# Kernel tuning notes

Measured on AMD Instinct MI355X. Metric: run time of the kernel, lower is better.

Reference implementation:

```python
import jax, jax.numpy as jnp
import numpy as np

N = 100_000   # total nodes in batch
E = 800_000   # total edges (avg degree ~8)
D = 128       # emb_dim
B = 1024      # graphs per batch
NT = 10       # num_tasks
EV = 4        # edge-type vocab
L_ENC = 5     # encoder GNN layers
L_RAT = 2     # rationale GNN layers
GAMMA = 0.4
BN_EPS = 1e-5


def setup_inputs() -> dict:
    keys = iter(jax.random.split(jax.random.key(0), 64))

    def nrm(shape, s=0.05):
        return jax.random.normal(next(keys), shape, jnp.float32) * s

    inp = {}
    inp["x"] = jax.random.normal(next(keys), (N, 4), jnp.float32)
    inp["edge_index"] = jax.random.randint(next(keys), (2, E), 0, N, jnp.int32)
    inp["edge_attr"] = jax.random.randint(next(keys), (E,), 0, EV, jnp.int32)
    inp["batch"] = jnp.sort(jax.random.randint(next(keys), (N,), 0, B, jnp.int32))
    inp["num_graphs"] = B
    u = jax.random.uniform(next(keys), (N, 2), jnp.float32, 1e-6, 1.0 - 1e-6)
    inp["gumbels"] = -jnp.log(-jnp.log(u))  # Gumbel(0,1) noise for gumbel_softmax

    inp["node_W"] = nrm((4, D)); inp["node_b"] = jnp.zeros((D,), jnp.float32)

    def gnn_params(L, pre):
        inp[pre + "eps"] = jnp.zeros((L,), jnp.float32)
        inp[pre + "edge"] = nrm((L, EV, D))
        inp[pre + "W1"] = nrm((L, D, 2 * D)); inp[pre + "b1"] = jnp.zeros((L, 2 * D), jnp.float32)
        inp[pre + "bn1g"] = jnp.ones((L, 2 * D), jnp.float32); inp[pre + "bn1b"] = jnp.zeros((L, 2 * D), jnp.float32)
        inp[pre + "W2"] = nrm((L, 2 * D, D)); inp[pre + "b2"] = jnp.zeros((L, D), jnp.float32)
        inp[pre + "bng"] = jnp.ones((L, D), jnp.float32); inp[pre + "bnb"] = jnp.zeros((L, D), jnp.float32)

    gnn_params(L_ENC, "enc_")
    gnn_params(L_RAT, "rat_")

    inp["gate_W1"] = nrm((D, 2 * D)); inp["gate_b1"] = jnp.zeros((2 * D,), jnp.float32)
    inp["gate_bng"] = jnp.ones((2 * D,), jnp.float32); inp["gate_bnb"] = jnp.zeros((2 * D,), jnp.float32)
    inp["gate_W2"] = nrm((2 * D, 2)); inp["gate_b2"] = jnp.zeros((2,), jnp.float32)

    inp["pred_W1"] = nrm((D, 2 * D)); inp["pred_b1"] = jnp.zeros((2 * D,), jnp.float32)
    inp["pred_bng"] = jnp.ones((2 * D,), jnp.float32); inp["pred_bnb"] = jnp.zeros((2 * D,), jnp.float32)
    inp["pred_W2"] = nrm((2 * D, NT)); inp["pred_b2"] = jnp.zeros((NT,), jnp.float32)
    return inp


def _bn(x, g, b):
    # training-mode BatchNorm1d: batch statistics over dim 0
    m = x.mean(0)
    v = x.var(0)
    return (x - m) * jax.lax.rsqrt(v + BN_EPS) * g + b


def _gin_stack(h, src, dst, ea, eps, edge, W1, b1, bn1g, bn1b, W2, b2, bng, bnb):
    # OGB-style GIN with edge embeddings, outer BN, residual
    n = h.shape[0]
    L = eps.shape[0]
    for l in range(L):
        msg = jax.nn.relu(h[src] + edge[l][ea])                 # [E, D] gather
        aggr = jax.ops.segment_sum(msg, dst, num_segments=n)    # scatter-add
        z = (1.0 + eps[l]) * h + aggr
        z = jax.nn.relu(_bn(z @ W1[l] + b1[l], bn1g[l], bn1b[l])) @ W2[l] + b2[l]
        z = _bn(z, bng[l], bnb[l])
        if l < L - 1:
            z = jax.nn.relu(z)
        h = z + h                                               # residual
    return h


def reference(x, gumbels, node_W, node_b,
              enc_eps, enc_edge, enc_W1, enc_b1, enc_bn1g, enc_bn1b, enc_W2, enc_b2, enc_bng, enc_bnb,
              rat_eps, rat_edge, rat_W1, rat_b1, rat_bn1g, rat_bn1b, rat_W2, rat_b2, rat_bng, rat_bnb,
              gate_W1, gate_b1, gate_bng, gate_bnb, gate_W2, gate_b2,
              pred_W1, pred_b1, pred_bng, pred_bnb, pred_W2, pred_b2,
              edge_index, edge_attr, batch, num_graphs):
    src, dst = edge_index[0], edge_index[1]
    h0 = x @ node_W + node_b                                    # node_enoder
    h_node = _gin_stack(h0, src, dst, edge_attr, enc_eps, enc_edge, enc_W1, enc_b1,
                        enc_bn1g, enc_bn1b, enc_W2, enc_b2, enc_bng, enc_bnb)
    xr = _gin_stack(h0, src, dst, edge_attr, rat_eps, rat_edge, rat_W1, rat_b1,
                    rat_bn1g, rat_bn1b, rat_W2, rat_b2, rat_bng, rat_bnb)

    # gate_nn: Linear -> BN -> ReLU -> (Dropout, eval) -> Linear
    logits = jax.nn.relu(_bn(xr @ gate_W1 + gate_b1, gate_bng, gate_bnb)) @ gate_W2 + gate_b2

    # F.gumbel_softmax(hard=True, tau=1) with straight-through estimator
    y_soft = jax.nn.softmax(logits + gumbels, axis=-1)
    y_hard = jax.nn.one_hot(jnp.argmax(y_soft, axis=-1), 2, dtype=y_soft.dtype)
    y = y_hard + y_soft - jax.lax.stop_gradient(y_soft)
    gate = y[:, 1:2]                                            # [N, 1]

    ones = jnp.ones((x.shape[0],), x.dtype)
    counts = jnp.maximum(jax.ops.segment_sum(ones, batch, num_segments=num_graphs), 1.0)[:, None]
    h_r = jax.ops.segment_sum(gate * h_node, batch, num_segments=num_graphs) / counts
    r_num = jax.ops.segment_sum(gate, batch, num_segments=num_graphs) + 1e-8
    env_num = jax.ops.segment_sum(1.0 - gate, batch, num_segments=num_graphs) + 1e-8

    pred_rem = jax.nn.relu(_bn(h_r @ pred_W1 + pred_b1, pred_bng, pred_bnb)) @ pred_W2 + pred_b2
    loss_reg = jnp.abs(r_num / (r_num + env_num) - GAMMA).mean()
    return pred_rem, loss_reg
```

## Files before the change

kernel.cpp:

```cpp
#include <hip/hip_runtime.h>
#include <cstddef>

#define DIM    128
#define DIM2   256
#define NGRAPH 1024
#define NTASK  10
#define NEV    4
#define BNEPS  1e-5f
#define GAMMA_ 0.4f

typedef __attribute__((ext_vector_type(4))) float f32x4;
typedef __attribute__((ext_vector_type(8))) short s16x8;

static __device__ __forceinline__ float relu_(float v) { return v > 0.f ? v : 0.f; }
static __device__ __forceinline__ unsigned short f2b(float f) {
    unsigned int u = __float_as_uint(f);
    unsigned int r = (u + 0x7fffu + ((u >> 16) & 1u)) >> 16;
    return (unsigned short)r;
}
static __device__ __forceinline__ float b2f(unsigned short b) {
    return __uint_as_float(((unsigned int)b) << 16);
}
static __device__ __forceinline__ unsigned int pk(float a, float b) {
    return (unsigned int)f2b(a) | ((unsigned int)f2b(b) << 16);
}

__global__ void k_count_deg(const int* __restrict__ dst, int* __restrict__ deg, int E) {
    int e = blockIdx.x * blockDim.x + threadIdx.x;
    if (e < E) atomicAdd(&deg[dst[e]], 1);
}

__global__ void k_scan_block(const int* __restrict__ deg, int* __restrict__ incl,
                             int* __restrict__ bsum, int n) {
    __shared__ int s[1024];
    int i = blockIdx.x * 1024 + threadIdx.x;
    int v = (i < n) ? deg[i] : 0;
    s[threadIdx.x] = v;
    __syncthreads();
    for (int off = 1; off < 1024; off <<= 1) {
        int t = (threadIdx.x >= off) ? s[threadIdx.x - off] : 0;
        __syncthreads();
        s[threadIdx.x] += t;
        __syncthreads();
    }
    if (i < n) incl[i] = s[threadIdx.x];
    if (threadIdx.x == 1023) bsum[blockIdx.x] = s[1023];
}

__global__ void k_scan_bsum(const int* __restrict__ bsum, int* __restrict__ boff, int nb) {
    __shared__ int s[128];
    int t = threadIdx.x;
    s[t] = (t < nb) ? bsum[t] : 0;
    __syncthreads();
    for (int off = 1; off < 128; off <<= 1) {
        int v = (t >= off) ? s[t - off] : 0;
        __syncthreads();
        s[t] += v;
        __syncthreads();
    }
    if (t < nb) boff[t] = (t == 0) ? 0 : s[t - 1];
}

__global__ void k_scan_final(const int* __restrict__ incl, const int* __restrict__ deg,
                             const int* __restrict__ boff, int* __restrict__ rowptr,
                             int* __restrict__ cursor, int n) {
    int i = blockIdx.x * blockDim.x + threadIdx.x;
    if (i < n) {
        int v = incl[i] + boff[i >> 10];
        rowptr[i + 1] = v;
        cursor[i] = v - deg[i];
    }
    if (i == 0) rowptr[0] = 0;
}

__global__ void k_fill_csr(const int* __restrict__ src, const int* __restrict__ dst,
                           const int* __restrict__ ea, int* __restrict__ cursor,
                           int* __restrict__ src_s, int* __restrict__ ea_s, int E) {
    int e = blockIdx.x * blockDim.x + threadIdx.x;
    if (e < E) {
        int p = atomicAdd(&cursor[dst[e]], 1);
        src_s[p] = src[e];
        ea_s[p]  = ea[e];
    }
}

__global__ void k_graph_ptr(const int* __restrict__ batch, int* __restrict__ gptr, int n, int B) {
    int g = blockIdx.x * blockDim.x + threadIdx.x;
    if (g > B) return;
    int lo = 0, hi = n;
    while (lo < hi) {
        int mid = (lo + hi) >> 1;
        if (batch[mid] < g) lo = mid + 1; else hi = mid;
    }
    gptr[g] = lo;
}

__global__ void k_wconv(const float* __restrict__ W, unsigned short* __restrict__ Wt,
                        int L, int K, int COUT) {
    long long i = (long long)blockIdx.x * 256 + threadIdx.x;
    long long total = (long long)L * K * COUT;
    if (i >= total) return;
    int l = (int)(i / (K * COUT));
    int rem = (int)(i % (K * COUT));
    int c = rem / K, k = rem % K;
    Wt[i] = f2b(W[(size_t)l * K * COUT + (size_t)k * COUT + c]);
}

__global__ void k_h0(const float* __restrict__ x, const float* __restrict__ W,
                     const float* __restrict__ b, float* __restrict__ h,
                     unsigned short* __restrict__ hb, int n) {
    int idx = blockIdx.x * blockDim.x + threadIdx.x;
    if (idx >= n * (DIM / 4)) return;
    int node = idx >> 5;
    int c4 = (idx & 31) << 2;
    const float* xr = x + (size_t)node * 4;
    float x0 = xr[0], x1 = xr[1], x2 = xr[2], x3 = xr[3];
    const float4 w0 = *(const float4*)(W + c4);
    const float4 w1 = *(const float4*)(W + DIM + c4);
    const float4 w2 = *(const float4*)(W + 2 * DIM + c4);
    const float4 w3 = *(const float4*)(W + 3 * DIM + c4);
    const float4 bv = *(const float4*)(b + c4);
    float4 o;
    o.x = bv.x + x0 * w0.x + x1 * w1.x + x2 * w2.x + x3 * w3.x;
    o.y = bv.y + x0 * w0.y + x1 * w1.y + x2 * w2.y + x3 * w3.y;
    o.z = bv.z + x0 * w0.z + x1 * w1.z + x2 * w2.z + x3 * w3.z;
    o.w = bv.w + x0 * w0.w + x1 * w1.w + x2 * w2.w + x3 * w3.w;
    size_t off = (size_t)node * DIM + c4;
    *(float4*)(h + off) = o;
    if (hb) {
        uint2 ob;
        ob.x = pk(o.x, o.y);
        ob.y = pk(o.z, o.w);
        *(uint2*)(hb + off) = ob;
    }
}

__global__ __launch_bounds__(256) void k_aggregate(
    const float* __restrict__ h, const int* __restrict__ rowptr,
    const int* __restrict__ src_s, const int* __restrict__ ea_s,
    const float* __restrict__ emb, const float* __restrict__ eps_arr, int l,
    float* __restrict__ zout, int n) {
    __shared__ float semb[NEV * DIM];
    int t = threadIdx.x;
    for (int i = t; i < NEV * DIM; i += 256) semb[i] = emb[(size_t)l * NEV * DIM + i];
    __syncthreads();
    int grp = t >> 5, lane = t & 31;
    int node = blockIdx.x * 8 + grp;
    if (node >= n) return;
    float eps1 = 1.0f + eps_arr[l];
    int beg = rowptr[node], end = rowptr[node + 1];
    int c = lane << 2;
    float4 acc = {0.f, 0.f, 0.f, 0.f};
    for (int e = beg; e < end; ++e) {
        int s = src_s[e];
        int a = ea_s[e];
        const float4 hv = *(const float4*)(h + (size_t)s * DIM + c);
        const float4 ev = *(const float4*)(semb + a * DIM + c);
        acc.x += relu_(hv.x + ev.x);
        acc.y += relu_(hv.y + ev.y);
        acc.z += relu_(hv.z + ev.z);
        acc.w += relu_(hv.w + ev.w);
    }
    const float4 hn = *(const float4*)(h + (size_t)node * DIM + c);
    float4 o;
    o.x = eps1 * hn.x + acc.x;
    o.y = eps1 * hn.y + acc.y;
    o.z = eps1 * hn.z + acc.z;
    o.w = eps1 * hn.w + acc.w;
    *(float4*)(zout + (size_t)node * DIM + c) = o;
}

__global__ __launch_bounds__(256) void k_agg_bf(
    const unsigned short* __restrict__ hb, const int* __restrict__ rowptr,
    const int* __restrict__ src_s, const int* __restrict__ ea_s,
    const float* __restrict__ emb, const float* __restrict__ eps_arr, int l,
    unsigned short* __restrict__ zb, int n) {
    __shared__ float semb[NEV * DIM];
    int t = threadIdx.x;
    for (int i = t; i < NEV * DIM; i += 256) semb[i] = emb[(size_t)l * NEV * DIM + i];
    __syncthreads();
    int grp = t >> 5, lane = t & 31;
    int node = blockIdx.x * 8 + grp;
    if (node >= n) return;
    float eps1 = 1.0f + eps_arr[l];
    int beg = rowptr[node], end = rowptr[node + 1];
    int c = lane << 2;
    float ax = 0.f, ay = 0.f, az = 0.f, aw = 0.f;
    for (int e = beg; e < end; ++e) {
        int s = src_s[e];
        int a = ea_s[e];
        ushort4 hv = *(const ushort4*)(hb + (size_t)s * DIM + c);
        const float4 ev = *(const float4*)(semb + a * DIM + c);
        ax += relu_(b2f(hv.x) + ev.x);
        ay += relu_(b2f(hv.y) + ev.y);
        az += relu_(b2f(hv.z) + ev.z);
        aw += relu_(b2f(hv.w) + ev.w);
    }
    ushort4 hn = *(const ushort4*)(hb + (size_t)node * DIM + c);
    uint2 o;
    o.x = pk(eps1 * b2f(hn.x) + ax, eps1 * b2f(hn.y) + ay);
    o.y = pk(eps1 * b2f(hn.z) + az, eps1 * b2f(hn.w) + aw);
    *(uint2*)(zb + (size_t)node * DIM + c) = o;
}

template <int K, int COUT, bool TRANS, bool STATS>
__global__ __launch_bounds__(256) void k_mmf(
    const float* __restrict__ A, const float* __restrict__ W,
    const float* __restrict__ bias, const float* __restrict__ scl,
    const float* __restrict__ shf, float* __restrict__ C,
    float* __restrict__ psum, float* __restrict__ psq, int nrows) {
    __shared__ float Asl[64][36];
    __shared__ float Wsl[32][132];
    const int t = threadIdx.x;
    const int row0 = blockIdx.x * 64;
    const int col0 = blockIdx.y * 128;
    const int tc = t & 15;
    const int tr = t >> 4;
    float4 acc[4][2] = {};
    for (int k0 = 0; k0 < K; k0 += 32) {
#pragma unroll
        for (int j = 0; j < 2; ++j) {
            int ff = j * 256 + t;
            int r = ff >> 3;
            int kc = (ff & 7) << 2;
            int grow = row0 + r;
            float4 v = {0.f, 0.f, 0.f, 0.f};
            if (grow < nrows) v = *(const float4*)(A + (size_t)grow * K + (k0 + kc));
            if (TRANS) {
                const float4 s4 = *(const float4*)(scl + k0 + kc);
                const float4 h4 = *(const float4*)(shf + k0 + kc);
                v.x = relu_(v.x * s4.x + h4.x);
                v.y = relu_(v.y * s4.y + h4.y);
                v.z = relu_(v.z * s4.z + h4.z);
                v.w = relu_(v.w * s4.w + h4.w);
            }
            *(float4*)(&Asl[r][kc]) = v;
        }
#pragma unroll
        for (int j = 0; j < 4; ++j) {
            int ff = j * 256 + t;
            int kr = ff >> 5;
            int cc = (ff & 31) << 2;
            float4 wv = *(const float4*)(W + (size_t)(k0 + kr) * COUT + (col0 + cc));
            *(float4*)(&Wsl[kr][cc]) = wv;
        }
        __syncthreads();
#pragma unroll
        for (int k4 = 0; k4 < 32; k4 += 4) {
            f32x4 a4[4];
#pragma unroll
            for (int r = 0; r < 4; ++r)
                a4[r] = *(const f32x4*)(&Asl[(tr << 2) + r][k4]);
#pragma unroll
            for (int kk = 0; kk < 4; ++kk) {
                const float4 w0 = *(const float4*)(&Wsl[k4 + kk][tc << 2]);
                const float4 w1 = *(const float4*)(&Wsl[k4 + kk][64 + (tc << 2)]);
                const float a0 = a4[0][kk];
                const float a1 = a4[1][kk];
                const float a2 = a4[2][kk];
                const float a3 = a4[3][kk];
                acc[0][0].x += a0 * w0.x; acc[0][0].y += a0 * w0.y; acc[0][0].z += a0 * w0.z; acc[0][0].w += a0 * w0.w;
                acc[0][1].x += a0 * w1.x; acc[0][1].y += a0 * w1.y; acc[0][1].z += a0 * w1.z; acc[0][1].w += a0 * w1.w;
                acc[1][0].x += a1 * w0.x; acc[1][0].y += a1 * w0.y; acc[1][0].z += a1 * w0.z; acc[1][0].w += a1 * w0.w;
                acc[1][1].x += a1 * w1.x; acc[1][1].y += a1 * w1.y; acc[1][1].z += a1 * w1.z; acc[1][1].w += a1 * w1.w;
                acc[2][0].x += a2 * w0.x; acc[2][0].y += a2 * w0.y; acc[2][0].z += a2 * w0.z; acc[2][0].w += a2 * w0.w;
                acc[2][1].x += a2 * w1.x; acc[2][1].y += a2 * w1.y; acc[2][1].z += a2 * w1.z; acc[2][1].w += a2 * w1.w;
                acc[3][0].x += a3 * w0.x; acc[3][0].y += a3 * w0.y; acc[3][0].z += a3 * w0.z; acc[3][0].w += a3 * w0.w;
                acc[3][1].x += a3 * w1.x; acc[3][1].y += a3 * w1.y; acc[3][1].z += a3 * w1.z; acc[3][1].w += a3 * w1.w;
            }
        }
        __syncthreads();
    }
    const float4 b0 = *(const float4*)(bias + col0 + (tc << 2));
    const float4 b1 = *(const float4*)(bias + col0 + 64 + (tc << 2));
    float s0[4] = {}, q0[4] = {}, s1[4] = {}, q1[4] = {};
#pragma unroll
    for (int r = 0; r < 4; ++r) {
        int row = row0 + (tr << 2) + r;
        if (row < nrows) {
            float4 o0, o1;
            o0.x = acc[r][0].x + b0.x; o0.y = acc[r][0].y + b0.y;
            o0.z = acc[r][0].z + b0.z; o0.w = acc[r][0].w + b0.w;
            o1.x = acc[r][1].x + b1.x; o1.y = acc[r][1].y + b1.y;
            o1.z = acc[r][1].z + b1.z; o1.w = acc[r][1].w + b1.w;
            *(float4*)(C + (size_t)row * COUT + col0 + (tc << 2)) = o0;
            *(float4*)(C + (size_t)row * COUT + col0 + 64 + (tc << 2)) = o1;
            if (STATS) {
                s0[0] += o0.x; q0[0] += o0.x * o0.x;  s0[1] += o0.y; q0[1] += o0.y * o0.y;
                s0[2] += o0.z; q0[2] += o0.z * o0.z;  s0[3] += o0.w; q0[3] += o0.w * o0.w;
                s1[0] += o1.x; q1[0] += o1.x * o1.x;  s1[1] += o1.y; q1[1] += o1.y * o1.y;
                s1[2] += o1.z; q1[2] += o1.z * o1.z;  s1[3] += o1.w; q1[3] += o1.w * o1.w;
            }
        }
    }
    if (STATS) {
        float* ls1 = &Wsl[0][0];
        float* ls2 = &Asl[0][0];
        __syncthreads();
#pragma unroll
        for (int j = 0; j < 4; ++j) {
            ls1[tr * 132 + (tc << 2) + j] = s0[j];
            ls1[tr * 132 + 64 + (tc << 2) + j] = s1[j];
            ls2[tr * 132 + (tc << 2) + j] = q0[j];
            ls2[tr * 132 + 64 + (tc << 2) + j] = q1[j];
        }
        __syncthreads();
        if (t < 128) {
            float ss = 0.f, qq = 0.f;
#pragma unroll
            for (int g = 0; g < 16; ++g) { ss += ls1[g * 132 + t]; qq += ls2[g * 132 + t]; }
            psum[(size_t)blockIdx.x * COUT + col0 + t] = ss;
            psq[(size_t)blockIdx.x * COUT + col0 + t]  = qq;
        }
    }
}

template <int K, int COUT, bool TRANS, bool OUT_BF, bool STATS>
__global__ __launch_bounds__(256) void k_mm_bf(
    const unsigned short* __restrict__ A, const unsigned short* __restrict__ Wt,
    const float* __restrict__ bias, const float* __restrict__ scl,
    const float* __restrict__ shf, void* __restrict__ Cout,
    float* __restrict__ psum, float* __restrict__ psq, int nrows) {
    __shared__ unsigned short As[128 * 64];
    __shared__ unsigned short Bs[64 * 64];
    const int t = threadIdx.x;
    const int row0 = blockIdx.x * 128;
    const int col0 = blockIdx.y * 64;
    const int wid = t >> 6, lane = t & 63;
    const int wm = wid & 1, wn = wid >> 1;
    const int lr = lane & 15, lk = lane >> 4;
    f32x4 acc[4][2] = {};
    for (int k0 = 0; k0 < K; k0 += 64) {
#pragma unroll
        for (int i = 0; i < 4; ++i) {
            int idx = i * 256 + t;
            int r = idx >> 3;
            int kc = (idx & 7) * 8;
            int gr = row0 + r;
            uint4 v = {0u, 0u, 0u, 0u};
            if (!TRANS) {
                if (gr < nrows) v = *(const uint4*)(A + (size_t)gr * K + k0 + kc);
            } else {
                if (gr < nrows) {
                    uint4 raw = *(const uint4*)(A + (size_t)gr * K + k0 + kc);
                    const float4 s0 = *(const float4*)(scl + k0 + kc);
                    const float4 s1 = *(const float4*)(scl + k0 + kc + 4);
                    const float4 h0 = *(const float4*)(shf + k0 + kc);
                    const float4 h1 = *(const float4*)(shf + k0 + kc + 4);
                    float v0 = relu_(b2f((unsigned short)(raw.x & 0xffff)) * s0.x + h0.x);
                    float v1 = relu_(b2f((unsigned short)(raw.x >> 16))    * s0.y + h0.y);
                    float v2 = relu_(b2f((unsigned short)(raw.y & 0xffff)) * s0.z + h0.z);
                    float v3 = relu_(b2f((unsigned short)(raw.y >> 16))    * s0.w + h0.w);
                    float v4 = relu_(b2f((unsigned short)(raw.z & 0xffff)) * s1.x + h1.x);
                    float v5 = relu_(b2f((unsigned short)(raw.z >> 16))    * s1.y + h1.y);
                    float v6 = relu_(b2f((unsigned short)(raw.w & 0xffff)) * s1.z + h1.z);
                    float v7 = relu_(b2f((unsigned short)(raw.w >> 16))    * s1.w + h1.w);
                    v.x = pk(v0, v1); v.y = pk(v2, v3); v.z = pk(v4, v5); v.w = pk(v6, v7);
                }
            }
            int byte = (r * 128 + kc * 2) ^ ((r & 7) << 4);
            *(uint4*)((char*)As + byte) = v;
        }
#pragma unroll
        for (int i = 0; i < 2; ++i) {
            int idx = i * 256 + t;
            int c = idx >> 3;
            int kc = (idx & 7) * 8;
            uint4 v = *(const uint4*)(Wt + (size_t)(col0 + c) * K + k0 + kc);
            int byte = (c * 128 + kc * 2) ^ ((c & 7) << 4);
            *(uint4*)((char*)Bs + byte) = v;
        }
        __syncthreads();
#pragma unroll
        for (int kk = 0; kk < 64; kk += 32) {
            s16x8 bfrag[2];
#pragma unroll
            for (int n = 0; n < 2; ++n) {
                int c = wn * 32 + n * 16 + lr;
                int byte = (c * 128 + (kk + lk * 8) * 2) ^ ((c & 7) << 4);
                bfrag[n] = *(const s16x8*)((const char*)Bs + byte);
            }
#pragma unroll
            for (int m = 0; m < 4; ++m) {
                int r = wm * 64 + m * 16 + lr;
                int byte = (r * 128 + (kk + lk * 8) * 2) ^ ((r & 7) << 4);
                s16x8 afrag = *(const s16x8*)((const char*)As + byte);
                acc[m][0] = __builtin_amdgcn_mfma_f32_16x16x32_bf16(afrag, bfrag[0], acc[m][0], 0, 0, 0);
                acc[m][1] = __builtin_amdgcn_mfma_f32_16x16x32_bf16(afrag, bfrag[1], acc[m][1], 0, 0, 0);
            }
        }
        __syncthreads();
    }
    float* ls1 = (float*)&Bs[0];
    float* ls2 = ls1 + 512;
#pragma unroll
    for (int n = 0; n < 2; ++n) {
        int col_local = wn * 32 + n * 16 + lr;
        int col = col0 + col_local;
        float bv = bias[col];
        float s = 0.f, q = 0.f;
#pragma unroll
        for (int m = 0; m < 4; ++m) {
#pragma unroll
            for (int j = 0; j < 4; ++j) {
                int row = row0 + wm * 64 + m * 16 + lk * 4 + j;
                if (row < nrows) {
                    float v = acc[m][n][j] + bv;
                    if (OUT_BF)
                        ((unsigned short*)Cout)[(size_t)row * COUT + col] = f2b(v);
                    else
                        ((float*)Cout)[(size_t)row * COUT + col] = v;
                    if (STATS) { s += v; q += v * v; }
                }
            }
        }
        if (STATS) {
            ls1[col_local * 8 + wm * 4 + lk] = s;
            ls2[col_local * 8 + wm * 4 + lk] = q;
        }
    }
    if (STATS) {
        __syncthreads();
        if (t < 64) {
            float ss = 0.f, qq = 0.f;
#pragma unroll
            for (int g = 0; g < 8; ++g) { ss += ls1[t * 8 + g]; qq += ls2[t * 8 + g]; }
            psum[(size_t)blockIdx.x * COUT + col0 + t] = ss;
            psq[(size_t)blockIdx.x * COUT + col0 + t]  = qq;
        }
    }
}

__global__ void k_stats_fin(const float* __restrict__ psum, const float* __restrict__ psq,
                            const float* __restrict__ g, const float* __restrict__ bta,
                            float* __restrict__ scl, float* __restrict__ shf,
                            int nrows, int C, int P) {
    __shared__ float r1[256], r2[256];
    int c = blockIdx.x;
    int t = threadIdx.x;
    float s = 0.f, sq = 0.f;
    for (int b = t; b < P; b += 256) {
        s  += psum[(size_t)b * C + c];
        sq += psq[(size_t)b * C + c];
    }
    r1[t] = s; r2[t] = sq;
    for (int off = 128; off; off >>= 1) {
        __syncthreads();
        if (t < off) { r1[t] += r1[t + off]; r2[t] += r2[t + off]; }
    }
    __syncthreads();
    if (t == 0) {
        float mean = r1[0] / (float)nrows;
        float var  = r2[0] / (float)nrows - mean * mean;
        float is   = rsqrtf(var + BNEPS);
        float sc   = g[c] * is;
        scl[c] = sc;
        shf[c] = bta[c] - mean * sc;
    }
}

__global__ void k_residual(const float* __restrict__ z, const float* __restrict__ scl,
                           const float* __restrict__ shf, float* __restrict__ h,
                           unsigned short* __restrict__ hb, int n, int relu_flag) {
    int idx = blockIdx.x * blockDim.x + threadIdx.x;
    if (idx >= n * (DIM / 4)) return;
    int i = idx * 4;
    int c = i & 127;
    const float4 zv = *(const float4*)(z + i);
    const float4 sv = *(const float4*)(scl + c);
    const float4 fv = *(const float4*)(shf + c);
    float4 hv = *(const float4*)(h + i);
    float v0 = zv.x * sv.x + fv.x;
    float v1 = zv.y * sv.y + fv.y;
    float v2 = zv.z * sv.z + fv.z;
    float v3 = zv.w * sv.w + fv.w;
    if (relu_flag) { v0 = relu_(v0); v1 = relu_(v1); v2 = relu_(v2); v3 = relu_(v3); }
    float4 o;
    o.x = v0 + hv.x; o.y = v1 + hv.y; o.z = v2 + hv.z; o.w = v3 + hv.w;
    *(float4*)(h + i) = o;
    if (hb) {
        uint2 ob;
        ob.x = pk(o.x, o.y);
        ob.y = pk(o.z, o.w);
        *(uint2*)(hb + i) = ob;
    }
}

__global__ __launch_bounds__(256) void k_gate(
    const float* __restrict__ t1, const float* __restrict__ scl, const float* __restrict__ shf,
    const float* __restrict__ W2, const float* __restrict__ b2,
    const float* __restrict__ gumbels, float* __restrict__ gate, int n) {
    __shared__ float w0[256], w1[256];
    int t = threadIdx.x;
    w0[t] = W2[t * 2];
    w1[t] = W2[t * 2 + 1];
    __syncthreads();
    int wv = t >> 6, lane = t & 63;
    int node = blockIdx.x * 4 + wv;
    if (node >= n) return;
    int c = lane << 2;
    const float4 v = *(const float4*)(t1 + (size_t)node * 256 + c);
    float a0 = 0.f, a1 = 0.f;
    float tv;
    tv = relu_(v.x * scl[c + 0] + shf[c + 0]); a0 += tv * w0[c + 0]; a1 += tv * w1[c + 0];
    tv = relu_(v.y * scl[c + 1] + shf[c + 1]); a0 += tv * w0[c + 1]; a1 += tv * w1[c + 1];
    tv = relu_(v.z * scl[c + 2] + shf[c + 2]); a0 += tv * w0[c + 2]; a1 += tv * w1[c + 2];
    tv = relu_(v.w * scl[c + 3] + shf[c + 3]); a0 += tv * w0[c + 3]; a1 += tv * w1[c + 3];
    for (int off = 32; off; off >>= 1) {
        a0 += __shfl_down(a0, off);
        a1 += __shfl_down(a1, off);
    }
    if (lane == 0) {
        float l0 = a0 + b2[0] + gumbels[(size_t)node * 2 + 0];
        float l1 = a1 + b2[1] + gumbels[(size_t)node * 2 + 1];
        gate[node] = (l1 > l0) ? 1.f : 0.f;
    }
}

__global__ void k_segreduce(const float* __restrict__ h, const float* __restrict__ gate,
                            const int* __restrict__ gptr, float* __restrict__ hr,
                            float* __restrict__ lossg, int B) {
    __shared__ float red[256];
    int g = blockIdx.x, t = threadIdx.x;
    int beg = gptr[g], end = gptr[g + 1];
    int cnt = end - beg;
    float gs = 0.f;
    for (int nrow = beg + t; nrow < end; nrow += 256) gs += gate[nrow];
    red[t] = gs;
    for (int off = 128; off; off >>= 1) {
        __syncthreads();
        if (t < off) red[t] += red[t + off];
    }
    __syncthreads();
    float rnum = red[0];
    __syncthreads();
    if (t == 0) {
        float r = rnum + 1e-8f;
        float e = ((float)cnt - rnum) + 1e-8f;
        lossg[g] = fabsf(r / (r + e) - GAMMA_);
    }
    int c = t & 127, rs = t >> 7;
    float acc = 0.f;
    for (int nrow = beg + rs; nrow < end; nrow += 2) {
        float gt = gate[nrow];
        if (gt != 0.f) acc += h[(size_t)nrow * 128 + c];
    }
    red[t] = acc;
    __syncthreads();
    if (rs == 0) {
        float tot = red[t] + red[t + 128];
        hr[(size_t)g * 128 + c] = tot / fmaxf((float)cnt, 1.f);
    }
}

__global__ void k_loss(const float* __restrict__ lossg, float* __restrict__ out, int B) {
    __shared__ float red[256];
    int t = threadIdx.x;
    float s = 0.f;
    for (int g = t; g < B; g += 256) s += lossg[g];
    red[t] = s;
    for (int off = 128; off; off >>= 1) {
        __syncthreads();
        if (t < off) red[t] += red[t + off];
    }
    __syncthreads();
    if (t == 0) out[NGRAPH * NTASK] = red[0] / (float)B;
}

__global__ void k_pred_out(const float* __restrict__ tp, const float* __restrict__ scl,
                           const float* __restrict__ shf, const float* __restrict__ W2,
                           const float* __restrict__ b2, float* __restrict__ out, int B) {
    int i = blockIdx.x * blockDim.x + threadIdx.x;
    if (i >= B * NTASK) return;
    int g = i / NTASK, j = i % NTASK;
    float acc = b2[j];
    for (int k = 0; k < 256; ++k) {
        float v = relu_(tp[(size_t)g * 256 + k] * scl[k] + shf[k]);
        acc += v * W2[k * NTASK + j];
    }
    out[i] = acc;
}

extern "C" void kernel_launch(void* const* d_in, const int* in_sizes, int n_in,
                              void* d_out, int out_size, void* d_ws, size_t ws_size,
                              hipStream_t stream) {
    const float* x       = (const float*)d_in[0];
    const int*   eidx    = (const int*)d_in[1];
    const int*   eattr   = (const int*)d_in[2];
    const int*   batch   = (const int*)d_in[3];
    const float* gumbels = (const float*)d_in[5];
    const float* node_W  = (const float*)d_in[6];
    const float* node_b  = (const float*)d_in[7];
    const float* enc_eps = (const float*)d_in[8];
    const float* enc_edge= (const float*)d_in[9];
    const float* enc_W1  = (const float*)d_in[10];
    const float* enc_b1  = (const float*)d_in[11];
    const float* enc_bn1g= (const float*)d_in[12];
    const float* enc_bn1b= (const float*)d_in[13];
    const float* enc_W2  = (const float*)d_in[14];
    const float* enc_b2  = (const float*)d_in[15];
    const float* enc_bng = (const float*)d_in[16];
    const float* enc_bnb = (const float*)d_in[17];
    const float* rat_eps = (const float*)d_in[18];
    const float* rat_edge= (const float*)d_in[19];
    const float* rat_W1  = (const float*)d_in[20];
    const float* rat_b1  = (const float*)d_in[21];
    const float* rat_bn1g= (const float*)d_in[22];
    const float* rat_bn1b= (const float*)d_in[23];
    const float* rat_W2  = (const float*)d_in[24];
    const float* rat_b2  = (const float*)d_in[25];
    const float* rat_bng = (const float*)d_in[26];
    const float* rat_bnb = (const float*)d_in[27];
    const float* gate_W1 = (const float*)d_in[28];
    const float* gate_b1 = (const float*)d_in[29];
    const float* gate_bng= (const float*)d_in[30];
    const float* gate_bnb= (const float*)d_in[31];
    const float* gate_W2 = (const float*)d_in[32];
    const float* gate_b2 = (const float*)d_in[33];
    const float* pred_W1 = (const float*)d_in[34];
    const float* pred_b1 = (const float*)d_in[35];
    const float* pred_bng= (const float*)d_in[36];
    const float* pred_bnb= (const float*)d_in[37];
    const float* pred_W2 = (const float*)d_in[38];
    const float* pred_b2 = (const float*)d_in[39];
    float* out = (float*)d_out;

    const int N = in_sizes[0] / 4;
    const int E = in_sizes[2];
    const int B = NGRAPH;

    const int gM64  = (N + 63) / 64;
    const int gM128 = (N + 127) / 128;

    char* w = (char*)d_ws;
    auto alloc = [&](size_t bytes) {
        char* p = w;
        w += (bytes + 255) & ~(size_t)255;
        return p;
    };
    float* h     = (float*)alloc((size_t)N * DIM * 4);
    float* buf   = (float*)alloc((size_t)N * DIM * 4);
    char*  t1base= alloc((size_t)N * DIM2 * 4);
    float* gate  = (float*)alloc((size_t)N * 4);
    float* scl   = (float*)alloc(256 * 4);
    float* shf   = (float*)alloc(256 * 4);
    float* psum  = (float*)alloc((size_t)gM64 * 256 * 4);
    float* psq   = (float*)alloc((size_t)gM64 * 256 * 4);
    float* hr    = (float*)alloc((size_t)B * DIM * 4);
    float* tpred = (float*)alloc((size_t)B * DIM2 * 4);
    float* lossg = (float*)alloc((size_t)B * 4);
    int* deg     = (int*)alloc((size_t)N * 4);
    int* incl    = (int*)alloc((size_t)N * 4);
    int* cursor  = (int*)alloc((size_t)N * 4);
    int* rowptr  = (int*)alloc((size_t)(N + 1) * 4);
    int* bsum    = (int*)alloc(128 * 4);
    int* boff    = (int*)alloc(128 * 4);
    int* srcs    = (int*)alloc((size_t)E * 4);
    int* eas     = (int*)alloc((size_t)E * 4);
    int* gptr    = (int*)alloc((size_t)(B + 1) * 4);
    unsigned short* W1t = (unsigned short*)alloc((size_t)5 * DIM2 * DIM * 2);
    unsigned short* W2t = (unsigned short*)alloc((size_t)5 * DIM * DIM2 * 2);

    float* t1          = (float*)t1base;
    unsigned short* zb  = (unsigned short*)t1base;
    unsigned short* t1b = (unsigned short*)(t1base + (size_t)N * DIM * 2);
    unsigned short* hb  = (unsigned short*)(t1base + (size_t)N * (DIM + DIM2) * 2);

    const int NB = (N + 1023) / 1024;

    hipMemsetAsync(deg, 0, (size_t)N * 4, stream);
    k_count_deg<<<(E + 255) / 256, 256, 0, stream>>>(eidx + E, deg, E);
    k_scan_block<<<NB, 1024, 0, stream>>>(deg, incl, bsum, N);
    k_scan_bsum<<<1, 128, 0, stream>>>(bsum, boff, NB);
    k_scan_final<<<(N + 255) / 256, 256, 0, stream>>>(incl, deg, boff, rowptr, cursor, N);
    k_fill_csr<<<(E + 255) / 256, 256, 0, stream>>>(eidx, eidx + E, eattr, cursor, srcs, eas, E);
    k_graph_ptr<<<(B + 256) / 256, 256, 0, stream>>>(batch, gptr, N, B);

    {
        long long tot1 = 5LL * DIM * DIM2;
        k_wconv<<<(int)((tot1 + 255) / 256), 256, 0, stream>>>(enc_W1, W1t, 5, DIM, DIM2);
        k_wconv<<<(int)((tot1 + 255) / 256), 256, 0, stream>>>(enc_W2, W2t, 5, DIM2, DIM);
    }

    const int gE4 = (N * (DIM / 4) + 255) / 256;

    k_h0<<<gE4, 256, 0, stream>>>(x, node_W, node_b, h, nullptr, N);
    for (int l = 0; l < 2; ++l) {
        k_aggregate<<<(N + 7) / 8, 256, 0, stream>>>(h, rowptr, srcs, eas, rat_edge, rat_eps, l, buf, N);
        k_mmf<128, 256, false, true><<<dim3(gM64, 2), 256, 0, stream>>>(
            buf, rat_W1 + (size_t)l * 128 * 256, rat_b1 + (size_t)l * 256, nullptr, nullptr,
            t1, psum, psq, N);
        k_stats_fin<<<256, 256, 0, stream>>>(psum, psq, rat_bn1g + (size_t)l * 256,
                                             rat_bn1b + (size_t)l * 256, scl, shf, N, 256, gM64);
        k_mmf<256, 128, true, true><<<dim3(gM64, 1), 256, 0, stream>>>(
            t1, rat_W2 + (size_t)l * 256 * 128, rat_b2 + (size_t)l * 128, scl, shf,
            buf, psum, psq, N);
        k_stats_fin<<<128, 256, 0, stream>>>(psum, psq, rat_bng + (size_t)l * 128,
                                             rat_bnb + (size_t)l * 128, scl, shf, N, 128, gM64);
        k_residual<<<gE4, 256, 0, stream>>>(buf, scl, shf, h, nullptr, N, (l < 1) ? 1 : 0);
    }
    k_mmf<128, 256, false, true><<<dim3(gM64, 2), 256, 0, stream>>>(
        h, gate_W1, gate_b1, nullptr, nullptr, t1, psum, psq, N);
    k_stats_fin<<<256, 256, 0, stream>>>(psum, psq, gate_bng, gate_bnb, scl, shf, N, 256, gM64);
    k_gate<<<(N + 3) / 4, 256, 0, stream>>>(t1, scl, shf, gate_W2, gate_b2, gumbels, gate, N);

    k_h0<<<gE4, 256, 0, stream>>>(x, node_W, node_b, h, hb, N);
    for (int l = 0; l < 5; ++l) {
        k_agg_bf<<<(N + 7) / 8, 256, 0, stream>>>(hb, rowptr, srcs, eas, enc_edge, enc_eps, l, zb, N);
        k_mm_bf<128, 256, false, true, true><<<dim3(gM128, 4), 256, 0, stream>>>(
            zb, W1t + (size_t)l * DIM2 * DIM, enc_b1 + (size_t)l * 256, nullptr, nullptr,
            t1b, psum, psq, N);
        k_stats_fin<<<256, 256, 0, stream>>>(psum, psq, enc_bn1g + (size_t)l * 256,
                                             enc_bn1b + (size_t)l * 256, scl, shf, N, 256, gM128);
        k_mm_bf<256, 128, true, false, true><<<dim3(gM128, 2), 256, 0, stream>>>(
            t1b, W2t + (size_t)l * DIM * DIM2, enc_b2 + (size_t)l * 128, scl, shf,
            buf, psum, psq, N);
        k_stats_fin<<<128, 256, 0, stream>>>(psum, psq, enc_bng + (size_t)l * 128,
                                             enc_bnb + (size_t)l * 128, scl, shf, N, 128, gM128);
        k_residual<<<gE4, 256, 0, stream>>>(buf, scl, shf, h, (l < 4) ? hb : nullptr, N, (l < 4) ? 1 : 0);
    }

    k_segreduce<<<B, 256, 0, stream>>>(h, gate, gptr, hr, lossg, B);
    k_loss<<<1, 256, 0, stream>>>(lossg, out, B);

    {
        const int gMB = (B + 63) / 64;
        k_mmf<128, 256, false, true><<<dim3(gMB, 2), 256, 0, stream>>>(
            hr, pred_W1, pred_b1, nullptr, nullptr, tpred, psum, psq, B);
        k_stats_fin<<<256, 256, 0, stream>>>(psum, psq, pred_bng, pred_bnb, scl, shf, B, 256, gMB);
        k_pred_out<<<(B * NTASK + 255) / 256, 256, 0, stream>>>(tpred, scl, shf, pred_W2,
                                                                pred_b2, out, B);
    }
}
```

Baseline: 1.808 ms.

## Use direct global-to-LDS loads with XOR swizzle and larger fp32 GEMM tiles

The fp32 GEMM now uses 128-row tiles with 8 rows per thread, and for the non-transform path it stages A and W straight into LDS through global_load_lds with an XOR-swizzled layout. The bf16 MFMA GEMM gets the same direct-to-LDS treatment for its non-transform A loads and all weight loads. The aim is to skip the register round-trip on tile staging, reduce bank conflicts, and raise arithmetic intensity per block. In exchange, register pressure rises from the doubled accumulators, there are fewer blocks in flight, and out-of-range rows are clamped rather than zero-filled.

```diff
diff --git a/kernel.cpp b/kernel.cpp
--- a/kernel.cpp
+++ b/kernel.cpp
@@ -209,64 +209,80 @@
     const float* __restrict__ bias, const float* __restrict__ scl,
     const float* __restrict__ shf, float* __restrict__ C,
     float* __restrict__ psum, float* __restrict__ psq, int nrows) {
-    __shared__ float Asl[64][36];
-    __shared__ float Wsl[32][132];
+    __shared__ float Asw[128 * 32];
+    __shared__ float Wsl[32 * 128];
     const int t = threadIdx.x;
-    const int row0 = blockIdx.x * 64;
+    const int lane = t & 63, wid = t >> 6;
+    const int row0 = blockIdx.x * 128;
     const int col0 = blockIdx.y * 128;
     const int tc = t & 15;
     const int tr = t >> 4;
-    float4 acc[4][2] = {};
+    float4 acc[8][2] = {};
     for (int k0 = 0; k0 < K; k0 += 32) {
-#pragma unroll
-        for (int j = 0; j < 2; ++j) {
-            int ff = j * 256 + t;
-            int r = ff >> 3;
-            int kc = (ff & 7) << 2;
-            int grow = row0 + r;
-            float4 v = {0.f, 0.f, 0.f, 0.f};
-            if (grow < nrows) v = *(const float4*)(A + (size_t)grow * K + (k0 + kc));
-            if (TRANS) {
-                const float4 s4 = *(const float4*)(scl + k0 + kc);
-                const float4 h4 = *(const float4*)(shf + k0 + kc);
-                v.x = relu_(v.x * s4.x + h4.x);
-                v.y = relu_(v.y * s4.y + h4.y);
-                v.z = relu_(v.z * s4.z + h4.z);
-                v.w = relu_(v.w * s4.w + h4.w);
-            }
-            *(float4*)(&Asl[r][kc]) = v;
-        }
-#pragma unroll
-        for (int j = 0; j < 4; ++j) {
-            int ff = j * 256 + t;
-            int kr = ff >> 5;
-            int cc = (ff & 31) << 2;
-            float4 wv = *(const float4*)(W + (size_t)(k0 + kr) * COUT + (col0 + cc));
-            *(float4*)(&Wsl[kr][cc]) = wv;
+        if (!TRANS) {
+#pragma unroll
+            for (int i = 0; i < 4; ++i) {
+                int g = i * 4 + wid;
+                int s = g * 64 + lane;
+                int r = s >> 3, c = s & 7;
+                int gr = row0 + r; if (gr >= nrows) gr = nrows - 1;
+                int cs = c ^ ((r & 7) ^ ((r >> 3) & 7));
+                const float* src = A + (size_t)gr * K + k0 + cs * 4;
+                __builtin_amdgcn_global_load_lds((const unsigned int*)src,
+                    (unsigned int*)((char*)Asw + g * 1024), 16, 0, 0);
+            }
+        } else {
+#pragma unroll
+            for (int j = 0; j < 4; ++j) {
+                int s = j * 256 + t;
+                int r = s >> 3;
+                int kc = (s & 7) << 2;
+                int gr = row0 + r;
+                float4 v = {0.f, 0.f, 0.f, 0.f};
+                if (gr < nrows) {
+                    v = *(const float4*)(A + (size_t)gr * K + k0 + kc);
+                    const float4 s4 = *(const float4*)(scl + k0 + kc);
+                    const float4 h4 = *(const float4*)(shf + k0 + kc);
+                    v.x = relu_(v.x * s4.x + h4.x);
+                    v.y = relu_(v.y * s4.y + h4.y);
+                    v.z = relu_(v.z * s4.z + h4.z);
+                    v.w = relu_(v.w * s4.w + h4.w);
+                }
+                int byte = (r * 128 + kc * 4) ^ ((((r & 7) ^ ((r >> 3) & 7))) << 4);
+                *(float4*)((char*)Asw + byte) = v;
+            }
+        }
+#pragma unroll
+        for (int i = 0; i < 4; ++i) {
+            int g = i * 4 + wid;
+            int s = g * 64 + lane;
+            int kr = s >> 5, c = s & 31;
+            const float* src = W + (size_t)(k0 + kr) * COUT + col0 + c * 4;
+            __builtin_amdgcn_global_load_lds((const unsigned int*)src,
+                (unsigned int*)((char*)Wsl + g * 1024), 16, 0, 0);
         }
         __syncthreads();
 #pragma unroll
         for (int k4 = 0; k4 < 32; k4 += 4) {
-            f32x4 a4[4];
-#pragma unroll
-            for (int r = 0; r < 4; ++r)
-                a4[r] = *(const f32x4*)(&Asl[(tr << 2) + r][k4]);
+            f32x4 a4[8];
+#pragma unroll
+            for (int rr = 0; rr < 8; ++rr) {
+                int r = tr * 8 + rr;
+                int byte = (r * 128 + (k4 >> 2) * 16) ^ ((((r & 7) ^ ((r >> 3) & 7))) << 4);
+                a4[rr] = *(const f32x4*)((const char*)Asw + byte);
+            }
 #pragma unroll
             for (int kk = 0; kk < 4; ++kk) {
-                const float4 w0 = *(const float4*)(&Wsl[k4 + kk][tc << 2]);
-                const float4 w1 = *(const float4*)(&Wsl[k4 + kk][64 + (tc << 2)]);
-                const float a0 = a4[0][kk];
-                const float a1 = a4[1][kk];
-                const float a2 = a4[2][kk];
-                const float a3 = a4[3][kk];
-                acc[0][0].x += a0 * w0.x; acc[0][0].y += a0 * w0.y; acc[0][0].z += a0 * w0.z; acc[0][0].w += a0 * w0.w;
-                acc[0][1].x += a0 * w1.x; acc[0][1].y += a0 * w1.y; acc[0][1].z += a0 * w1.z; acc[0][1].w += a0 * w1.w;
-                acc[1][0].x += a1 * w0.x; acc[1][0].y += a1 * w0.y; acc[1][0].z += a1 * w0.z; acc[1][0].w += a1 * w0.w;
-                acc[1][1].x += a1 * w1.x; acc[1][1].y += a1 * w1.y; acc[1][1].z += a1 * w1.z; acc[1][1].w += a1 * w1.w;
-                acc[2][0].x += a2 * w0.x; acc[2][0].y += a2 * w0.y; acc[2][0].z += a2 * w0.z; acc[2][0].w += a2 * w0.w;
-                acc[2][1].x += a2 * w1.x; acc[2][1].y += a2 * w1.y; acc[2][1].z += a2 * w1.z; acc[2][1].w += a2 * w1.w;
-                acc[3][0].x += a3 * w0.x; acc[3][0].y += a3 * w0.y; acc[3][0].z += a3 * w0.z; acc[3][0].w += a3 * w0.w;
-                acc[3][1].x += a3 * w1.x; acc[3][1].y += a3 * w1.y; acc[3][1].z += a3 * w1.z; acc[3][1].w += a3 * w1.w;
+                const float4 w0 = *(const float4*)(Wsl + (k4 + kk) * 128 + (tc << 2));
+                const float4 w1 = *(const float4*)(Wsl + (k4 + kk) * 128 + 64 + (tc << 2));
+#pragma unroll
+                for (int rr = 0; rr < 8; ++rr) {
+                    float a = a4[rr][kk];
+                    acc[rr][0].x += a * w0.x; acc[rr][0].y += a * w0.y;
+                    acc[rr][0].z += a * w0.z; acc[rr][0].w += a * w0.w;
+                    acc[rr][1].x += a * w1.x; acc[rr][1].y += a * w1.y;
+                    acc[rr][1].z += a * w1.z; acc[rr][1].w += a * w1.w;
+                }
             }
         }
         __syncthreads();
@@ -275,14 +291,14 @@
     const float4 b1 = *(const float4*)(bias + col0 + 64 + (tc << 2));
     float s0[4] = {}, q0[4] = {}, s1[4] = {}, q1[4] = {};
 #pragma unroll
-    for (int r = 0; r < 4; ++r) {
-        int row = row0 + (tr << 2) + r;
+    for (int rr = 0; rr < 8; ++rr) {
+        int row = row0 + tr * 8 + rr;
         if (row < nrows) {
             float4 o0, o1;
-            o0.x = acc[r][0].x + b0.x; o0.y = acc[r][0].y + b0.y;
-            o0.z = acc[r][0].z + b0.z; o0.w = acc[r][0].w + b0.w;
-            o1.x = acc[r][1].x + b1.x; o1.y = acc[r][1].y + b1.y;
-            o1.z = acc[r][1].z + b1.z; o1.w = acc[r][1].w + b1.w;
+            o0.x = acc[rr][0].x + b0.x; o0.y = acc[rr][0].y + b0.y;
+            o0.z = acc[rr][0].z + b0.z; o0.w = acc[rr][0].w + b0.w;
+            o1.x = acc[rr][1].x + b1.x; o1.y = acc[rr][1].y + b1.y;
+            o1.z = acc[rr][1].z + b1.z; o1.w = acc[rr][1].w + b1.w;
             *(float4*)(C + (size_t)row * COUT + col0 + (tc << 2)) = o0;
             *(float4*)(C + (size_t)row * COUT + col0 + 64 + (tc << 2)) = o1;
             if (STATS) {
@@ -294,21 +310,21 @@
         }
     }
     if (STATS) {
-        float* ls1 = &Wsl[0][0];
-        float* ls2 = &Asl[0][0];
+        float* ls1 = Wsl;
+        float* ls2 = Asw;
         __syncthreads();
 #pragma unroll
         for (int j = 0; j < 4; ++j) {
-            ls1[tr * 132 + (tc << 2) + j] = s0[j];
-            ls1[tr * 132 + 64 + (tc << 2) + j] = s1[j];
-            ls2[tr * 132 + (tc << 2) + j] = q0[j];
-            ls2[tr * 132 + 64 + (tc << 2) + j] = q1[j];
+            ls1[tr * 128 + (tc << 2) + j] = s0[j];
+            ls1[tr * 128 + 64 + (tc << 2) + j] = s1[j];
+            ls2[tr * 128 + (tc << 2) + j] = q0[j];
+            ls2[tr * 128 + 64 + (tc << 2) + j] = q1[j];
         }
         __syncthreads();
         if (t < 128) {
             float ss = 0.f, qq = 0.f;
 #pragma unroll
-            for (int g = 0; g < 16; ++g) { ss += ls1[g * 132 + t]; qq += ls2[g * 132 + t]; }
+            for (int g = 0; g < 16; ++g) { ss += ls1[g * 128 + t]; qq += ls2[g * 128 + t]; }
             psum[(size_t)blockIdx.x * COUT + col0 + t] = ss;
             psq[(size_t)blockIdx.x * COUT + col0 + t]  = qq;
         }
@@ -331,16 +347,26 @@
     const int lr = lane & 15, lk = lane >> 4;
     f32x4 acc[4][2] = {};
     for (int k0 = 0; k0 < K; k0 += 64) {
-#pragma unroll
-        for (int i = 0; i < 4; ++i) {
-            int idx = i * 256 + t;
-            int r = idx >> 3;
-            int kc = (idx & 7) * 8;
-            int gr = row0 + r;
-            uint4 v = {0u, 0u, 0u, 0u};
-            if (!TRANS) {
-                if (gr < nrows) v = *(const uint4*)(A + (size_t)gr * K + k0 + kc);
-            } else {
+        if (!TRANS) {
+#pragma unroll
+            for (int i = 0; i < 4; ++i) {
+                int g = i * 4 + wid;
+                int s = g * 64 + lane;
+                int r = s >> 3, c = s & 7;
+                int gr = row0 + r; if (gr >= nrows) gr = nrows - 1;
+                int cs = c ^ (r & 7);
+                const unsigned short* src = A + (size_t)gr * K + k0 + (cs << 3);
+                __builtin_amdgcn_global_load_lds((const unsigned int*)src,
+                    (unsigned int*)((char*)As + g * 1024), 16, 0, 0);
+            }
+        } else {
+#pragma unroll
+            for (int i = 0; i < 4; ++i) {
+                int idx = i * 256 + t;
+                int r = idx >> 3;
+                int kc = (idx & 7) * 8;
+                int gr = row0 + r;
+                uint4 v = {0u, 0u, 0u, 0u};
                 if (gr < nrows) {
                     uint4 raw = *(const uint4*)(A + (size_t)gr * K + k0 + kc);
                     const float4 s0 = *(const float4*)(scl + k0 + kc);
@@ -357,18 +383,19 @@
                     float v7 = relu_(b2f((unsigned short)(raw.w >> 16))    * s1.w + h1.w);
                     v.x = pk(v0, v1); v.y = pk(v2, v3); v.z = pk(v4, v5); v.w = pk(v6, v7);
                 }
-            }
-            int byte = (r * 128 + kc * 2) ^ ((r & 7) << 4);
-            *(uint4*)((char*)As + byte) = v;
+                int byte = (r * 128 + kc * 2) ^ ((r & 7) << 4);
+                *(uint4*)((char*)As + byte) = v;
+            }
         }
 #pragma unroll
         for (int i = 0; i < 2; ++i) {
-            int idx = i * 256 + t;
-            int c = idx >> 3;
-            int kc = (idx & 7) * 8;
-            uint4 v = *(const uint4*)(Wt + (size_t)(col0 + c) * K + k0 + kc);
-            int byte = (c * 128 + kc * 2) ^ ((c & 7) << 4);
-            *(uint4*)((char*)Bs + byte) = v;
+            int g = i * 4 + wid;
+            int s = g * 64 + lane;
+            int c = s >> 3, kc = s & 7;
+            int ks = kc ^ (c & 7);
+            const unsigned short* src = Wt + (size_t)(col0 + c) * K + k0 + (ks << 3);
+            __builtin_amdgcn_global_load_lds((const unsigned int*)src,
+                (unsigned int*)((char*)Bs + g * 1024), 16, 0, 0);
         }
         __syncthreads();
 #pragma unroll
@@ -629,7 +656,6 @@
     const int E = in_sizes[2];
     const int B = NGRAPH;
 
-    const int gM64  = (N + 63) / 64;
     const int gM128 = (N + 127) / 128;
 
     char* w = (char*)d_ws;
@@ -644,8 +670,8 @@
     float* gate  = (float*)alloc((size_t)N * 4);
     float* scl   = (float*)alloc(256 * 4);
     float* shf   = (float*)alloc(256 * 4);
-    float* psum  = (float*)alloc((size_t)gM64 * 256 * 4);
-    float* psq   = (float*)alloc((size_t)gM64 * 256 * 4);
+    float* psum  = (float*)alloc((size_t)gM128 * 256 * 4);
+    float* psq   = (float*)alloc((size_t)gM128 * 256 * 4);
     float* hr    = (float*)alloc((size_t)B * DIM * 4);
     float* tpred = (float*)alloc((size_t)B * DIM2 * 4);
     float* lossg = (float*)alloc((size_t)B * 4);
@@ -687,21 +713,21 @@
     k_h0<<<gE4, 256, 0, stream>>>(x, node_W, node_b, h, nullptr, N);
     for (int l = 0; l < 2; ++l) {
         k_aggregate<<<(N + 7) / 8, 256, 0, stream>>>(h, rowptr, srcs, eas, rat_edge, rat_eps, l, buf, N);
-        k_mmf<128, 256, false, true><<<dim3(gM64, 2), 256, 0, stream>>>(
+        k_mmf<128, 256, false, true><<<dim3(gM128, 2), 256, 0, stream>>>(
             buf, rat_W1 + (size_t)l * 128 * 256, rat_b1 + (size_t)l * 256, nullptr, nullptr,
             t1, psum, psq, N);
         k_stats_fin<<<256, 256, 0, stream>>>(psum, psq, rat_bn1g + (size_t)l * 256,
-                                             rat_bn1b + (size_t)l * 256, scl, shf, N, 256, gM64);
-        k_mmf<256, 128, true, true><<<dim3(gM64, 1), 256, 0, stream>>>(
+                                             rat_bn1b + (size_t)l * 256, scl, shf, N, 256, gM128);
+        k_mmf<256, 128, true, true><<<dim3(gM128, 1), 256, 0, stream>>>(
             t1, rat_W2 + (size_t)l * 256 * 128, rat_b2 + (size_t)l * 128, scl, shf,
             buf, psum, psq, N);
         k_stats_fin<<<128, 256, 0, stream>>>(psum, psq, rat_bng + (size_t)l * 128,
-                                             rat_bnb + (size_t)l * 128, scl, shf, N, 128, gM64);
+                                             rat_bnb + (size_t)l * 128, scl, shf, N, 128, gM128);
         k_residual<<<gE4, 256, 0, stream>>>(buf, scl, shf, h, nullptr, N, (l < 1) ? 1 : 0);
     }
-    k_mmf<128, 256, false, true><<<dim3(gM64, 2), 256, 0, stream>>>(
+    k_mmf<128, 256, false, true><<<dim3(gM128, 2), 256, 0, stream>>>(
         h, gate_W1, gate_b1, nullptr, nullptr, t1, psum, psq, N);
-    k_stats_fin<<<256, 256, 0, stream>>>(psum, psq, gate_bng, gate_bnb, scl, shf, N, 256, gM64);
+    k_stats_fin<<<256, 256, 0, stream>>>(psum, psq, gate_bng, gate_bnb, scl, shf, N, 256, gM128);
     k_gate<<<(N + 3) / 4, 256, 0, stream>>>(t1, scl, shf, gate_W2, gate_b2, gumbels, gate, N);
 
     k_h0<<<gE4, 256, 0, stream>>>(x, node_W, node_b, h, hb, N);
@@ -724,7 +750,7 @@
     k_loss<<<1, 256, 0, stream>>>(lossg, out, B);
 
     {
-        const int gMB = (B + 63) / 64;
+        const int gMB = (B + 127) / 128;
         k_mmf<128, 256, false, true><<<dim3(gMB, 2), 256, 0, stream>>>(
             hr, pred_W1, pred_b1, nullptr, nullptr, tpred, psum, psq, B);
         k_stats_fin<<<256, 256, 0, stream>>>(psum, psq, pred_bng, pred_bnb, scl, shf, B, 256, gMB);
```

Measured after the change: 2.033 ms. +12.4%, slower.

## Prefetch fp32 GEMM tiles into registers and use direct global-to-LDS loads for bf16 GEMM

Applied to the files above, without the earlier changes.

The fp32 k_mmf kernel now loads the next K-slice of A and W into registers while the current slice is being computed, and stores them to LDS at the start of each iteration. This software pipelining is meant to hide global-load latency. The bf16 MFMA kernel's non-transformed A tiles and its W tiles now use global_load_lds, which writes straight into LDS. The XOR swizzle is applied on the source address, so the shared-memory layout stays the same and the register staging round trip is skipped. Out-of-range rows are clamped to the last row rather than zero-filled. This relies on those rows being discarded at output time, and adds register pressure in the fp32 kernel.

```diff
diff --git a/kernel.cpp b/kernel.cpp
--- a/kernel.cpp
+++ b/kernel.cpp
@@ -217,34 +217,55 @@
     const int tc = t & 15;
     const int tr = t >> 4;
     float4 acc[4][2] = {};
-    for (int k0 = 0; k0 < K; k0 += 32) {
+    float4 ra[2], rw[4];
+
+    const int a_r0 = t >> 3;
+    const int a_kc = (t & 7) << 2;
+    const int w_kr0 = t >> 5;
+    const int w_cc = (t & 31) << 2;
+
+    auto loadA = [&](int k0) {
 #pragma unroll
         for (int j = 0; j < 2; ++j) {
-            int ff = j * 256 + t;
-            int r = ff >> 3;
-            int kc = (ff & 7) << 2;
+            int r = a_r0 + j * 32;
             int grow = row0 + r;
             float4 v = {0.f, 0.f, 0.f, 0.f};
-            if (grow < nrows) v = *(const float4*)(A + (size_t)grow * K + (k0 + kc));
-            if (TRANS) {
-                const float4 s4 = *(const float4*)(scl + k0 + kc);
-                const float4 h4 = *(const float4*)(shf + k0 + kc);
-                v.x = relu_(v.x * s4.x + h4.x);
-                v.y = relu_(v.y * s4.y + h4.y);
-                v.z = relu_(v.z * s4.z + h4.z);
-                v.w = relu_(v.w * s4.w + h4.w);
+            if (grow < nrows) {
+                v = *(const float4*)(A + (size_t)grow * K + k0 + a_kc);
+                if (TRANS) {
+                    const float4 s4 = *(const float4*)(scl + k0 + a_kc);
+                    const float4 h4 = *(const float4*)(shf + k0 + a_kc);
+                    v.x = relu_(v.x * s4.x + h4.x);
+                    v.y = relu_(v.y * s4.y + h4.y);
+                    v.z = relu_(v.z * s4.z + h4.z);
+                    v.w = relu_(v.w * s4.w + h4.w);
+                }
             }
-            *(float4*)(&Asl[r][kc]) = v;
-        }
+            ra[j] = v;
+        }
+    };
+    auto loadW = [&](int k0) {
 #pragma unroll
         for (int j = 0; j < 4; ++j) {
-            int ff = j * 256 + t;
-            int kr = ff >> 5;
-            int cc = (ff & 31) << 2;
-            float4 wv = *(const float4*)(W + (size_t)(k0 + kr) * COUT + (col0 + cc));
-            *(float4*)(&Wsl[kr][cc]) = wv;
-        }
-        __syncthreads();
+            int kr = w_kr0 + j * 8;
+            rw[j] = *(const float4*)(W + (size_t)(k0 + kr) * COUT + col0 + w_cc);
+        }
+    };
+    auto storeLDS = [&]() {
+#pragma unroll
+        for (int j = 0; j < 2; ++j)
+            *(float4*)(&Asl[a_r0 + j * 32][a_kc]) = ra[j];
+#pragma unroll
+        for (int j = 0; j < 4; ++j)
+            *(float4*)(&Wsl[w_kr0 + j * 8][w_cc]) = rw[j];
+    };
+
+    loadA(0);
+    loadW(0);
+    for (int k0 = 0; k0 < K; k0 += 32) {
+        storeLDS();
+        __syncthreads();
+        if (k0 + 32 < K) { loadA(k0 + 32); loadW(k0 + 32); }
 #pragma unroll
         for (int k4 = 0; k4 < 32; k4 += 4) {
             f32x4 a4[4];
@@ -331,16 +352,26 @@
     const int lr = lane & 15, lk = lane >> 4;
     f32x4 acc[4][2] = {};
     for (int k0 = 0; k0 < K; k0 += 64) {
-#pragma unroll
-        for (int i = 0; i < 4; ++i) {
-            int idx = i * 256 + t;
-            int r = idx >> 3;
-            int kc = (idx & 7) * 8;
-            int gr = row0 + r;
-            uint4 v = {0u, 0u, 0u, 0u};
-            if (!TRANS) {
-                if (gr < nrows) v = *(const uint4*)(A + (size_t)gr * K + k0 + kc);
-            } else {
+        if (!TRANS) {
+#pragma unroll
+            for (int i = 0; i < 4; ++i) {
+                int g = i * 4 + wid;
+                int s = g * 64 + lane;
+                int r = s >> 3, c = s & 7;
+                int gr = row0 + r; if (gr >= nrows) gr = nrows - 1;
+                int cs = c ^ (r & 7);
+                const unsigned short* src = A + (size_t)gr * K + k0 + (cs << 3);
+                __builtin_amdgcn_global_load_lds((const unsigned int*)src,
+                    (unsigned int*)((char*)As + g * 1024), 16, 0, 0);
+            }
+        } else {
+#pragma unroll
+            for (int i = 0; i < 4; ++i) {
+                int idx = i * 256 + t;
+                int r = idx >> 3;
+                int kc = (idx & 7) * 8;
+                int gr = row0 + r;
+                uint4 v = {0u, 0u, 0u, 0u};
                 if (gr < nrows) {
                     uint4 raw = *(const uint4*)(A + (size_t)gr * K + k0 + kc);
                     const float4 s0 = *(const float4*)(scl + k0 + kc);
@@ -357,18 +388,19 @@
                     float v7 = relu_(b2f((unsigned short)(raw.w >> 16))    * s1.w + h1.w);
                     v.x = pk(v0, v1); v.y = pk(v2, v3); v.z = pk(v4, v5); v.w = pk(v6, v7);
                 }
+                int byte = (r * 128 + kc * 2) ^ ((r & 7) << 4);
+                *(uint4*)((char*)As + byte) = v;
             }
-            int byte = (r * 128 + kc * 2) ^ ((r & 7) << 4);
-            *(uint4*)((char*)As + byte) = v;
         }
 #pragma unroll
         for (int i = 0; i < 2; ++i) {
-            int idx = i * 256 + t;
-            int c = idx >> 3;
-            int kc = (idx & 7) * 8;
-            uint4 v = *(const uint4*)(Wt + (size_t)(col0 + c) * K + k0 + kc);
-            int byte = (c * 128 + kc * 2) ^ ((c & 7) << 4);
-            *(uint4*)((char*)Bs + byte) = v;
+            int g = i * 4 + wid;
+            int s = g * 64 + lane;
+            int c = s >> 3, kc = s & 7;
+            int ks = kc ^ (c & 7);
+            const unsigned short* src = Wt + (size_t)(col0 + c) * K + k0 + (ks << 3);
+            __builtin_amdgcn_global_load_lds((const unsigned int*)src,
+                (unsigned int*)((char*)Bs + g * 1024), 16, 0, 0);
         }
         __syncthreads();
 #pragma unroll
```

Result: slower. 1.858 ms (+2.7%).
